# Kernel tuning notes

Hardware: AMD Instinct MI355X
Metric: run time of the kernel (lower is better)

## Reference

```python
import jax, jax.numpy as jnp
import numpy as np

B, HW, C, HEADS = 8, 64, 256, 8
H_SP, W_SP = 64, 8  # idx=0: horizontal stripe windows
L = HW * HW


def setup_inputs() -> dict:
    key = jax.random.key(0)
    k1, k2, k3 = jax.random.split(key, 3)
    qkv = jax.random.normal(k1, (3, B, L, C), dtype=jnp.float32)
    lepe_w = jax.random.normal(k2, (C, 1, 3, 3), dtype=jnp.float32) * 0.1
    lepe_b = jax.random.normal(k3, (C,), dtype=jnp.float32) * 0.01
    return {"qkv": qkv, "lepe_w": lepe_w, "lepe_b": lepe_b}


def _to_windows(x):
    # (B, L, C) -> (B*nWin, heads, H_sp*W_sp, head_dim)
    hd = C // HEADS
    x = x.reshape(B, HW // H_SP, H_SP, HW // W_SP, W_SP, C)
    x = x.transpose(0, 1, 3, 2, 4, 5).reshape(-1, H_SP * W_SP, HEADS, hd)
    return x.transpose(0, 2, 1, 3)


def reference(qkv, lepe_w, lepe_b):
    hd = C // HEADS
    scale = hd ** -0.5
    q, k, v = qkv[0], qkv[1], qkv[2]

    qw = _to_windows(q) * scale            # (W, h, T, d)
    kw = _to_windows(k)

    # v as window images (B*nWin, C, H_sp, W_sp) for depthwise LePE conv
    vim = v.reshape(B, HW // H_SP, H_SP, HW // W_SP, W_SP, C)
    vim = vim.transpose(0, 1, 3, 5, 2, 4).reshape(-1, C, H_SP, W_SP)
    lepe = jax.lax.conv_general_dilated(
        vim, lepe_w, window_strides=(1, 1), padding='SAME',
        feature_group_count=C,
        dimension_numbers=('NCHW', 'OIHW', 'NCHW'))
    lepe = lepe + lepe_b[None, :, None, None]

    def chw_to_heads(x):
        # (W, C, H_sp, W_sp) -> (W, heads, T, head_dim)
        return x.reshape(-1, HEADS, hd, H_SP * W_SP).transpose(0, 1, 3, 2)

    vw = chw_to_heads(vim)
    lp = chw_to_heads(lepe)

    attn = jax.nn.softmax(jnp.einsum('whqd,whkd->whqk', qw, kw), axis=-1)
    out = jnp.einsum('whqk,whkd->whqd', attn, vw) + lp   # (W, h, T, d)

    # merge windows back to (B, L, C)
    out = out.transpose(0, 2, 1, 3).reshape(-1, H_SP * W_SP, C)
    out = out.reshape(B, HW // H_SP, HW // W_SP, H_SP, W_SP, C)
    out = out.transpose(0, 1, 3, 2, 4, 5).reshape(B, L, C)
    return out, attn
```

## Files before the change

### kernel.cpp

```cpp
#include <hip/hip_runtime.h>

constexpr int Bc     = 8;
constexpr int HWc    = 64;
constexpr int Cc     = 256;
constexpr int HEADSc = 8;
constexpr int HDc    = 32;
constexpr int WSP    = 8;
constexpr int Tc     = 512;
constexpr int NWB    = 8;
constexpr int Lc     = 4096;

constexpr int QTILE = 128;
constexpr int NQT   = Tc / QTILE;

using f32x4  = __attribute__((ext_vector_type(4))) float;
using bf16x8 = __attribute__((ext_vector_type(8))) __bf16;

union F8 { uint4 q; bf16x8 b; };

__device__ __forceinline__ unsigned short f2b(float f) {
    unsigned u = __builtin_bit_cast(unsigned, f);
    unsigned r = (u + 0x7FFFu + ((u >> 16) & 1u)) >> 16;
    return (unsigned short)r;
}
__device__ __forceinline__ float b2f(unsigned short s) {
    unsigned u = ((unsigned)s) << 16;
    return __builtin_bit_cast(float, u);
}

constexpr int OFF_K  = 0;
constexpr int OFF_V  = 32768;
constexpr int OFF_PF = 65536;
constexpr int SMEM_BYTES = 81920;

__device__ __forceinline__ int swz64(int row, int byteoff) {
    return (row * 64 + byteoff) ^ ((row & 7) << 4);
}
__device__ __forceinline__ int swzV(int d, int byteoff) {
    return (d * 1024 + byteoff) ^ ((d & 7) << 4);
}
__device__ __forceinline__ int swz128(int row, int byteoff) {
    return row * 128 + (byteoff ^ ((row & 7) << 4));
}

__global__ __launch_bounds__(512, 4)
void lepe_attn_mfma(const float* __restrict__ qkv,
                    const float* __restrict__ lepe_w,
                    const float* __restrict__ lepe_b,
                    float* __restrict__ out,
                    float* __restrict__ attn)
{
    __shared__ __align__(16) unsigned char smem[SMEM_BYTES];

    const int i    = blockIdx.x;
    const int work = (i & 7) * (2048 / 8) + (i >> 3);
    const int qt   = work & (NQT - 1);
    const int wh   = work >> 2;
    const int h    = wh & (HEADSc - 1);
    const int w    = wh >> 3;
    const int b    = w >> 3;
    const int wb   = w & (NWB - 1);
    const int q0   = qt * QTILE;

    const int tid  = threadIdx.x;
    const int wave = tid >> 6;
    const int lane = tid & 63;

    const size_t planeBL = (size_t)Bc * Lc * Cc;
    const float* qb = qkv + (size_t)b * Lc * Cc;
    const float* kb = qb + planeBL;
    const float* vb = qb + 2 * planeBL;
    const int cbase = h * HDc;
    const float scale = 0.17677669529663687f;

    auto lofs = [&](int t) -> int { return (t >> 3) * HWc + wb * WSP + (t & 7); };

    const int q  = lane & 15;
    const int hh = lane >> 4;

    F8 qa;
    {
        const float* qsrc = qb + (size_t)lofs(q0 + wave * 16 + q) * Cc + cbase + hh * 8;
        float4 a = *(const float4*)qsrc;
        float4 c = *(const float4*)(qsrc + 4);
        unsigned short* us = (unsigned short*)&qa.q;
        us[0]=f2b(a.x*scale); us[1]=f2b(a.y*scale); us[2]=f2b(a.z*scale); us[3]=f2b(a.w*scale);
        us[4]=f2b(c.x*scale); us[5]=f2b(c.y*scale); us[6]=f2b(c.z*scale); us[7]=f2b(c.w*scale);
    }

    {
        const float* src = kb + (size_t)lofs(tid) * Cc + cbase;
        #pragma unroll
        for (int g2 = 0; g2 < 4; ++g2) {
            float4 a = *(const float4*)(src + g2 * 8);
            float4 c = *(const float4*)(src + g2 * 8 + 4);
            F8 u;
            unsigned short* us = (unsigned short*)&u.q;
            us[0]=f2b(a.x); us[1]=f2b(a.y); us[2]=f2b(a.z); us[3]=f2b(a.w);
            us[4]=f2b(c.x); us[5]=f2b(c.y); us[6]=f2b(c.z); us[7]=f2b(c.w);
            *(uint4*)(smem + OFF_K + swz64(tid, g2 * 16)) = u.q;
        }
    }
    {
        const int d0 = (tid & 7) * 4, g = tid >> 3;
        float4 ld[8];
        #pragma unroll
        for (int kk = 0; kk < 8; ++kk)
            ld[kk] = *(const float4*)(vb + (size_t)lofs(g * 8 + kk) * Cc + cbase + d0);
        #pragma unroll
        for (int m = 0; m < 4; ++m) {
            F8 u;
            unsigned short* us = (unsigned short*)&u.q;
            const float vals[8] = {ld[0].x, ld[0].y, ld[0].z, ld[0].w,
                                   ld[4].x, ld[4].y, ld[4].z, ld[4].w};
            us[0]=f2b((&ld[0].x)[m]); us[1]=f2b((&ld[1].x)[m]);
            us[2]=f2b((&ld[2].x)[m]); us[3]=f2b((&ld[3].x)[m]);
            us[4]=f2b((&ld[4].x)[m]); us[5]=f2b((&ld[5].x)[m]);
            us[6]=f2b((&ld[6].x)[m]); us[7]=f2b((&ld[7].x)[m]);
            (void)vals;
            *(uint4*)(smem + OFF_V + swzV(d0 + m, 16 * g)) = u.q;
        }
    }
    __syncthreads();

    float s = 0.f;
    #pragma unroll
    for (int f = 0; f < 32; ++f) {
        F8 kf; kf.q = *(const uint4*)(smem + OFF_K + swz64(16 * f + q, hh * 16));
        f32x4 t = __builtin_amdgcn_mfma_f32_16x16x32_bf16(kf.b, qa.b, (f32x4){0.f,0.f,0.f,0.f}, 0, 0, 0);
        s += __expf(t[0]) + __expf(t[1]) + __expf(t[2]) + __expf(t[3]);
    }
    s += __shfl_xor(s, 16);
    s += __shfl_xor(s, 32);
    const float ri = 1.0f / s;

    unsigned char* myPF = smem + OFF_PF + wave * 2048;
    float* arow0 = attn + ((size_t)wh * Tc + q0 + wave * 16) * Tc;

    f32x4 O[2] = {(f32x4){0.f,0.f,0.f,0.f}, (f32x4){0.f,0.f,0.f,0.f}};
    #pragma unroll
    for (int c = 0; c < 16; ++c) {
        F8 k0; k0.q = *(const uint4*)(smem + OFF_K + swz64(16 * (2*c)   + q, hh * 16));
        F8 k1; k1.q = *(const uint4*)(smem + OFF_K + swz64(16 * (2*c+1) + q, hh * 16));
        f32x4 t0 = __builtin_amdgcn_mfma_f32_16x16x32_bf16(k0.b, qa.b, (f32x4){0.f,0.f,0.f,0.f}, 0, 0, 0);
        f32x4 t1 = __builtin_amdgcn_mfma_f32_16x16x32_bf16(k1.b, qa.b, (f32x4){0.f,0.f,0.f,0.f}, 0, 0, 0);
        f32x4 p0, p1;
        #pragma unroll
        for (int j = 0; j < 4; ++j) { p0[j] = __expf(t0[j]) * ri; p1[j] = __expf(t1[j]) * ri; }

        *(f32x4*)(myPF + swz128(q, 16 * hh))      = p0;
        *(f32x4*)(myPF + swz128(q, 64 + 16 * hh)) = p1;

        #pragma unroll
        for (int half = 0; half < 2; ++half) {
            const int r = half * 8 + (lane >> 3);
            f32x4 vv = *(const f32x4*)(myPF + swz128(r, (lane & 7) * 16));
            __builtin_nontemporal_store(vv,
                (f32x4*)(arow0 + (size_t)r * Tc + 32 * c + (lane & 7) * 4));
        }

        F8 pa;
        {
            f32x4 ra = *(const f32x4*)(myPF + swz128(q, (32 * hh) ^ ((q & 7) << 4)) );
            f32x4 rb = *(const f32x4*)(myPF + swz128(q, (32 * hh + 16) ^ ((q & 7) << 4)) );
            ra = *(const f32x4*)(myPF + swz128(q, 32 * hh));
            rb = *(const f32x4*)(myPF + swz128(q, 32 * hh + 16));
            unsigned short* us = (unsigned short*)&pa.q;
            us[0]=f2b(ra[0]); us[1]=f2b(ra[1]); us[2]=f2b(ra[2]); us[3]=f2b(ra[3]);
            us[4]=f2b(rb[0]); us[5]=f2b(rb[1]); us[6]=f2b(rb[2]); us[7]=f2b(rb[3]);
        }

        #pragma unroll
        for (int hf = 0; hf < 2; ++hf) {
            const int d = q + 16 * hf;
            F8 vf; vf.q = *(const uint4*)(smem + OFF_V + swzV(d, 64 * c + 16 * hh));
            O[hf] = __builtin_amdgcn_mfma_f32_16x16x32_bf16(pa.b, vf.b, O[hf], 0, 0, 0);
        }
    }

    const int tok0 = q0 + wave * 16 + hh * 4;
    const int hi  = tok0 >> 3;
    const int wi0 = tok0 & 7;
    #pragma unroll
    for (int hf = 0; hf < 2; ++hf) {
        const int d  = q + 16 * hf;
        const int cg = cbase + d;
        float wv[9];
        #pragma unroll
        for (int t = 0; t < 9; ++t) wv[t] = lepe_w[(size_t)cg * 9 + t];
        const float bias = lepe_b[cg];

        uint4 vrow[3];
        #pragma unroll
        for (int dh = 0; dh < 3; ++dh) {
            const int nh = hi + dh - 1;
            vrow[dh] = ((unsigned)nh < (unsigned)HWc)
                     ? *(const uint4*)(smem + OFF_V + swzV(d, 16 * nh))
                     : make_uint4(0, 0, 0, 0);
        }

        #pragma unroll
        for (int j = 0; j < 4; ++j) {
            const int wi = wi0 + j;
            float lp = bias;
            #pragma unroll
            for (int dh = 0; dh < 3; ++dh) {
                const unsigned short* us = (const unsigned short*)&vrow[dh];
                #pragma unroll
                for (int dw = -1; dw <= 1; ++dw) {
                    const int wc = wi + dw;
                    if ((unsigned)wc < (unsigned)WSP)
                        lp += b2f(us[wc]) * wv[dh * 3 + (dw + 1)];
                }
            }
            __builtin_nontemporal_store(O[hf][j] + lp,
                out + ((size_t)b * Lc + lofs(tok0 + j)) * Cc + cg);
        }
    }
}

extern "C" void kernel_launch(void* const* d_in, const int* in_sizes, int n_in,
                              void* d_out, int out_size, void* d_ws, size_t ws_size,
                              hipStream_t stream) {
    const float* qkv = (const float*)d_in[0];
    const float* lw  = (const float*)d_in[1];
    const float* lb  = (const float*)d_in[2];
    float* out  = (float*)d_out;
    float* attn = out + (size_t)Bc * Lc * Cc;

    dim3 grid(64 * HEADSc * NQT);
    dim3 block(512);
    hipLaunchKernelGGL(lepe_attn_mfma, grid, block, 0, stream,
                       qkv, lw, lb, out, attn);
}
```

Measured before the change: 136.4 us.

## Cache unnormalized exp scores as packed bf16 in registers, defer normalization

The first QK^T pass now keeps exp(scores) packed into bf16 pairs in 64 registers, so the second pass no longer recomputes the QK MFMAs and exponentials. Normalization is deferred: attention rows are scaled by a shuffled reciprocal when written out, and the PV accumulator is scaled once at the end. The per-wave staging buffer shrinks to bf16, which halves its LDS footprint and lets the MFMA A-operand be read directly without conversion. The cost is higher register pressure, and the stored attention probabilities now carry bf16 rounding before normalization, which lowers their precision.

```diff
diff --git a/kernel.cpp b/kernel.cpp
--- a/kernel.cpp
+++ b/kernel.cpp
@@ -27,20 +27,28 @@
     unsigned u = ((unsigned)s) << 16;
     return __builtin_bit_cast(float, u);
 }
-
-constexpr int OFF_K  = 0;
-constexpr int OFF_V  = 32768;
-constexpr int OFF_PF = 65536;
-constexpr int SMEM_BYTES = 81920;
+__device__ __forceinline__ float b2f_lo(unsigned u) {
+    return __builtin_bit_cast(float, u << 16);
+}
+__device__ __forceinline__ float b2f_hi(unsigned u) {
+    return __builtin_bit_cast(float, u & 0xFFFF0000u);
+}
+__device__ __forceinline__ unsigned cvt_pk(float lo, float hi) {
+    unsigned r;
+    asm("v_cvt_pk_bf16_f32 %0, %1, %2" : "=v"(r) : "v"(lo), "v"(hi));
+    return r;
+}
+
+constexpr int OFF_K = 0;
+constexpr int OFF_V = 32768;
+constexpr int OFF_P = 65536;
+constexpr int SMEM_BYTES = 73728;
 
 __device__ __forceinline__ int swz64(int row, int byteoff) {
     return (row * 64 + byteoff) ^ ((row & 7) << 4);
 }
 __device__ __forceinline__ int swzV(int d, int byteoff) {
     return (d * 1024 + byteoff) ^ ((d & 7) << 4);
-}
-__device__ __forceinline__ int swz128(int row, int byteoff) {
-    return row * 128 + (byteoff ^ ((row & 7) << 4));
 }
 
 __global__ __launch_bounds__(512, 4)
@@ -111,64 +119,57 @@
         for (int m = 0; m < 4; ++m) {
             F8 u;
             unsigned short* us = (unsigned short*)&u.q;
-            const float vals[8] = {ld[0].x, ld[0].y, ld[0].z, ld[0].w,
-                                   ld[4].x, ld[4].y, ld[4].z, ld[4].w};
             us[0]=f2b((&ld[0].x)[m]); us[1]=f2b((&ld[1].x)[m]);
             us[2]=f2b((&ld[2].x)[m]); us[3]=f2b((&ld[3].x)[m]);
             us[4]=f2b((&ld[4].x)[m]); us[5]=f2b((&ld[5].x)[m]);
             us[6]=f2b((&ld[6].x)[m]); us[7]=f2b((&ld[7].x)[m]);
-            (void)vals;
             *(uint4*)(smem + OFF_V + swzV(d0 + m, 16 * g)) = u.q;
         }
     }
     __syncthreads();
 
     float s = 0.f;
+    unsigned Sb[64];
     #pragma unroll
     for (int f = 0; f < 32; ++f) {
         F8 kf; kf.q = *(const uint4*)(smem + OFF_K + swz64(16 * f + q, hh * 16));
         f32x4 t = __builtin_amdgcn_mfma_f32_16x16x32_bf16(kf.b, qa.b, (f32x4){0.f,0.f,0.f,0.f}, 0, 0, 0);
-        s += __expf(t[0]) + __expf(t[1]) + __expf(t[2]) + __expf(t[3]);
+        float e0 = __expf(t[0]), e1 = __expf(t[1]), e2 = __expf(t[2]), e3 = __expf(t[3]);
+        s += (e0 + e1) + (e2 + e3);
+        Sb[2 * f]     = cvt_pk(e0, e1);
+        Sb[2 * f + 1] = cvt_pk(e2, e3);
     }
     s += __shfl_xor(s, 16);
     s += __shfl_xor(s, 32);
     const float ri = 1.0f / s;
 
-    unsigned char* myPF = smem + OFF_PF + wave * 2048;
+    const float ri_a = __shfl(ri, (lane >> 3));
+    const float ri_b = __shfl(ri, 8 + (lane >> 3));
+    float ri_o[4];
+    #pragma unroll
+    for (int j = 0; j < 4; ++j) ri_o[j] = __shfl(ri, 4 * hh + j);
+
+    unsigned char* myP = smem + OFF_P + wave * 1024;
     float* arow0 = attn + ((size_t)wh * Tc + q0 + wave * 16) * Tc;
 
     f32x4 O[2] = {(f32x4){0.f,0.f,0.f,0.f}, (f32x4){0.f,0.f,0.f,0.f}};
     #pragma unroll
     for (int c = 0; c < 16; ++c) {
-        F8 k0; k0.q = *(const uint4*)(smem + OFF_K + swz64(16 * (2*c)   + q, hh * 16));
-        F8 k1; k1.q = *(const uint4*)(smem + OFF_K + swz64(16 * (2*c+1) + q, hh * 16));
-        f32x4 t0 = __builtin_amdgcn_mfma_f32_16x16x32_bf16(k0.b, qa.b, (f32x4){0.f,0.f,0.f,0.f}, 0, 0, 0);
-        f32x4 t1 = __builtin_amdgcn_mfma_f32_16x16x32_bf16(k1.b, qa.b, (f32x4){0.f,0.f,0.f,0.f}, 0, 0, 0);
-        f32x4 p0, p1;
-        #pragma unroll
-        for (int j = 0; j < 4; ++j) { p0[j] = __expf(t0[j]) * ri; p1[j] = __expf(t1[j]) * ri; }
-
-        *(f32x4*)(myPF + swz128(q, 16 * hh))      = p0;
-        *(f32x4*)(myPF + swz128(q, 64 + 16 * hh)) = p1;
+        *(uint2*)(myP + swz64(q, 8 * hh))      = make_uint2(Sb[4 * c],     Sb[4 * c + 1]);
+        *(uint2*)(myP + swz64(q, 32 + 8 * hh)) = make_uint2(Sb[4 * c + 2], Sb[4 * c + 3]);
 
         #pragma unroll
         for (int half = 0; half < 2; ++half) {
             const int r = half * 8 + (lane >> 3);
-            f32x4 vv = *(const f32x4*)(myPF + swz128(r, (lane & 7) * 16));
+            const float rr = half ? ri_b : ri_a;
+            uint2 u = *(const uint2*)(myP + swz64(r, 8 * (lane & 7)));
+            f32x4 vv = { b2f_lo(u.x) * rr, b2f_hi(u.x) * rr,
+                         b2f_lo(u.y) * rr, b2f_hi(u.y) * rr };
             __builtin_nontemporal_store(vv,
-                (f32x4*)(arow0 + (size_t)r * Tc + 32 * c + (lane & 7) * 4));
-        }
-
-        F8 pa;
-        {
-            f32x4 ra = *(const f32x4*)(myPF + swz128(q, (32 * hh) ^ ((q & 7) << 4)) );
-            f32x4 rb = *(const f32x4*)(myPF + swz128(q, (32 * hh + 16) ^ ((q & 7) << 4)) );
-            ra = *(const f32x4*)(myPF + swz128(q, 32 * hh));
-            rb = *(const f32x4*)(myPF + swz128(q, 32 * hh + 16));
-            unsigned short* us = (unsigned short*)&pa.q;
-            us[0]=f2b(ra[0]); us[1]=f2b(ra[1]); us[2]=f2b(ra[2]); us[3]=f2b(ra[3]);
-            us[4]=f2b(rb[0]); us[5]=f2b(rb[1]); us[6]=f2b(rb[2]); us[7]=f2b(rb[3]);
-        }
+                (f32x4*)(arow0 + (size_t)r * Tc + 32 * c + 4 * (lane & 7)));
+        }
+
+        F8 pa; pa.q = *(const uint4*)(myP + swz64(q, 16 * hh));
 
         #pragma unroll
         for (int hf = 0; hf < 2; ++hf) {
@@ -213,7 +214,7 @@
                         lp += b2f(us[wc]) * wv[dh * 3 + (dw + 1)];
                 }
             }
-            __builtin_nontemporal_store(O[hf][j] + lp,
+            __builtin_nontemporal_store(O[hf][j] * ri_o[j] + lp,
                 out + ((size_t)b * Lc + lofs(tok0 + j)) * Cc + cg);
         }
     }
```

New measurement: 131.2 us. -3.8%, faster.
